# Kernel optimization log

Measured on AMD Instinct MI355X. Metric: run time of the kernel, lower is better.

The kernel has to match this reference:

```python
import jax, jax.numpy as jnp
import numpy as np

EPS = 1e-12          # matches torch F.normalize eps
NOW = 3600.0         # fixed 'current time'; timestamps are in [0,1)
TIME_DECAY = 3600.0  # temporal decay constant from the module

def setup_inputs() -> dict:
    key = jax.random.key(0)
    k1, k2, k3, k4, k5 = jax.random.split(key, 5)
    M, D, S = 100000, 768, 2
    return {
        "query_features": jax.random.normal(k1, (D,), dtype=jnp.float32),
        "location": jax.random.normal(k2, (S,), dtype=jnp.float32),
        "memory_features": jax.random.normal(k3, (M, D), dtype=jnp.float32),
        "memory_locations": jax.random.normal(k4, (M, S), dtype=jnp.float32),
        "memory_metadata": jax.random.uniform(k5, (M, 4), dtype=jnp.float32),
        "k": 5,
    }

def reference(query_features, location, memory_features, memory_locations, memory_metadata, k):
    # --- cosine similarity: normalize query and memory rows (F.normalize semantics) ---
    q_norm = query_features / jnp.maximum(jnp.linalg.norm(query_features), EPS)      # [D]
    m_norms = jnp.maximum(jnp.linalg.norm(memory_features, axis=1, keepdims=True), EPS)
    m_norm = memory_features / m_norms                                               # [M, D]
    sim_scores = m_norm @ q_norm                                                     # [M] GEMV

    # --- spatial score: 1 / (1 + euclidean distance to query location) ---
    dists = jnp.linalg.norm(memory_locations - location[None, :], axis=1)            # [M]
    spatial_scores = 1.0 / (1.0 + dists)

    # --- temporal score: exp(-age / 3600) ---
    strengths = memory_metadata[:, 0]
    timestamps = memory_metadata[:, 1]
    ages = NOW - timestamps
    temporal_scores = jnp.exp(-ages / TIME_DECAY)

    combined = (0.5 * sim_scores + 0.3 * spatial_scores + 0.2 * temporal_scores) * strengths

    top_scores, top_indices = jax.lax.top_k(combined, k)
    return top_scores, top_indices
```

## Files before the change

kernel.cpp:

```cpp
#include <hip/hip_runtime.h>
#include <math.h>

#define EPS   1e-12f
#define NOW_T 3600.0f
#define TDEC  3600.0f
#define K     5
#define D     768
#define GRID  2048

__device__ __forceinline__ void consider(float (&v)[K], int (&ix)[K], float s, int i)
{
    if (s > v[K - 1]) {
        int j = K - 1;
        #pragma unroll
        for (int t = K - 1; t > 0; --t) {
            if (v[t - 1] < s) { v[t] = v[t - 1]; ix[t] = ix[t - 1]; j = t - 1; }
        }
        v[j] = s; ix[j] = i;
    }
}

__global__ __launch_bounds__(256) void score_topk_kernel(
    const float* __restrict__ q,
    const float* __restrict__ loc,
    const float* __restrict__ feat,
    const float* __restrict__ mloc,
    const float* __restrict__ meta,
    float* __restrict__ cand_val,
    int*   __restrict__ cand_idx,
    int M)
{
    const int tid = threadIdx.x;
    const int c   = tid & 15;
    const int g   = tid >> 4;

    const float* qp = q + c * 4;
    float4 qv[12];
    float qss = 0.f;
    #pragma unroll
    for (int j = 0; j < 12; ++j) {
        qv[j] = *(const float4*)(qp + j * 64);
        qss = fmaf(qv[j].x, qv[j].x, qss);
        qss = fmaf(qv[j].y, qv[j].y, qss);
        qss = fmaf(qv[j].z, qv[j].z, qss);
        qss = fmaf(qv[j].w, qv[j].w, qss);
    }
    #pragma unroll
    for (int m = 1; m < 16; m <<= 1) qss += __shfl_xor(qss, m);
    const float inv_qn = 1.0f / fmaxf(sqrtf(qss), EPS);

    const float lx = loc[0];
    const float ly = loc[1];

    float v[K]; int ix[K];
    #pragma unroll
    for (int j = 0; j < K; ++j) { v[j] = -INFINITY; ix[j] = -1; }

    for (int base = blockIdx.x * 16; base < M; base += GRID * 16) {
        const int row = base + g;
        float dot = 0.f, ss = 0.f;
        if (row < M) {
            const float* r = feat + (size_t)row * D + c * 4;
            #pragma unroll
            for (int j = 0; j < 12; ++j) {
                float4 f = *(const float4*)(r + j * 64);
                dot = fmaf(f.x, qv[j].x, dot); ss = fmaf(f.x, f.x, ss);
                dot = fmaf(f.y, qv[j].y, dot); ss = fmaf(f.y, f.y, ss);
                dot = fmaf(f.z, qv[j].z, dot); ss = fmaf(f.z, f.z, ss);
                dot = fmaf(f.w, qv[j].w, dot); ss = fmaf(f.w, f.w, ss);
            }
        }
        #pragma unroll
        for (int m = 1; m < 16; m <<= 1) {
            dot += __shfl_xor(dot, m);
            ss  += __shfl_xor(ss,  m);
        }
        if (row < M && c == 0) {
            float sim = dot * inv_qn / fmaxf(sqrtf(ss), EPS);
            float2 ml = *(const float2*)(mloc + (size_t)row * 2);
            float4 md = *(const float4*)(meta + (size_t)row * 4);
            float dx = ml.x - lx, dy = ml.y - ly;
            float dist = sqrtf(dx * dx + dy * dy);
            float spatial  = 1.0f / (1.0f + dist);
            float temporal = expf((md.y - NOW_T) / TDEC);
            float s = (0.5f * sim + 0.3f * spatial + 0.2f * temporal) * md.x;
            consider(v, ix, s, row);
        }
    }

    __shared__ float sv[16 * K];
    __shared__ int   si[16 * K];
    if (c == 0) {
        #pragma unroll
        for (int j = 0; j < K; ++j) { sv[g * K + j] = v[j]; si[g * K + j] = ix[j]; }
    }
    __syncthreads();
    if (tid == 0) {
        float bv[K]; int bi[K];
        #pragma unroll
        for (int j = 0; j < K; ++j) { bv[j] = -INFINITY; bi[j] = -1; }
        for (int t = 0; t < 16 * K; ++t) consider(bv, bi, sv[t], si[t]);
        #pragma unroll
        for (int j = 0; j < K; ++j) {
            cand_val[blockIdx.x * K + j] = bv[j];
            cand_idx[blockIdx.x * K + j] = bi[j];
        }
    }
}

__global__ __launch_bounds__(1024) void merge_kernel(
    const float* __restrict__ cand_val, const int* __restrict__ cand_idx,
    int N, float* __restrict__ out)
{
    __shared__ float s_val[1024 * K];
    __shared__ int   s_idx[1024 * K];

    const int tid = threadIdx.x;
    float v[K]; int ix[K];
    #pragma unroll
    for (int j = 0; j < K; ++j) { v[j] = -INFINITY; ix[j] = -1; }

    for (int i = tid; i < N; i += 1024)
        consider(v, ix, cand_val[i], cand_idx[i]);

    #pragma unroll
    for (int j = 0; j < K; ++j) { s_val[tid * K + j] = v[j]; s_idx[tid * K + j] = ix[j]; }
    __syncthreads();

    for (int sz = 1024 >> 1; sz >= 1; sz >>= 1) {
        if (tid < sz) {
            const float* pv = &s_val[(tid + sz) * K];
            const int*   pi = &s_idx[(tid + sz) * K];
            float mv[K]; int mi[K];
            int a = 0, b = 0;
            #pragma unroll
            for (int j = 0; j < K; ++j) {
                bool takeA = (b >= K) || (a < K && v[a] >= pv[b]);
                if (takeA) { mv[j] = v[a];  mi[j] = ix[a]; ++a; }
                else       { mv[j] = pv[b]; mi[j] = pi[b]; ++b; }
            }
            #pragma unroll
            for (int j = 0; j < K; ++j) {
                v[j] = mv[j]; ix[j] = mi[j];
                s_val[tid * K + j] = v[j]; s_idx[tid * K + j] = ix[j];
            }
        }
        __syncthreads();
    }

    if (tid == 0) {
        #pragma unroll
        for (int j = 0; j < K; ++j) {
            out[j]     = v[j];
            out[K + j] = (float)ix[j];
        }
    }
}

extern "C" void kernel_launch(void* const* d_in, const int* in_sizes, int n_in,
                              void* d_out, int out_size, void* d_ws, size_t ws_size,
                              hipStream_t stream) {
    const float* q    = (const float*)d_in[0];
    const float* loc  = (const float*)d_in[1];
    const float* feat = (const float*)d_in[2];
    const float* mloc = (const float*)d_in[3];
    const float* meta = (const float*)d_in[4];
    const int M = in_sizes[2] / D;

    float* cand_val = (float*)d_ws;
    int*   cand_idx = (int*)((char*)d_ws + GRID * K * sizeof(float));

    score_topk_kernel<<<GRID, 256, 0, stream>>>(q, loc, feat, mloc, meta,
                                                cand_val, cand_idx, M);
    merge_kernel<<<1, 1024, 0, stream>>>(cand_val, cand_idx, GRID * K, (float*)d_out);
}
```

Before: 434.3 us.

## Fuse merge into scoring kernel via last-block atomic, contiguous row ranges, nontemporal loads

Folds the separate single-block merge kernel into the scoring kernel. Each block bumps an atomic counter when it finishes, and the last block to finish merges all candidates. Each block now scans a contiguous range of rows instead of a grid-strided set, and feature rows are read with nontemporal loads. The aim is to drop the second kernel launch and its dependency gap and to improve streaming from DRAM. In exchange it adds a memset per call and a serial merge tail on one 256-thread block.

After: 465.9 us. +7.3%, slower.

```diff
diff --git a/kernel.cpp b/kernel.cpp
--- a/kernel.cpp
+++ b/kernel.cpp
@@ -7,6 +7,8 @@
 #define K     5
 #define D     768
 #define GRID  2048
+
+typedef float vfloat4 __attribute__((ext_vector_type(4)));
 
 __device__ __forceinline__ void consider(float (&v)[K], int (&ix)[K], float s, int i)
 {
@@ -20,7 +22,7 @@
     }
 }
 
-__global__ __launch_bounds__(256) void score_topk_kernel(
+__global__ __launch_bounds__(256) void fused_kernel(
     const float* __restrict__ q,
     const float* __restrict__ loc,
     const float* __restrict__ feat,
@@ -28,6 +30,8 @@
     const float* __restrict__ meta,
     float* __restrict__ cand_val,
     int*   __restrict__ cand_idx,
+    unsigned* __restrict__ done_ctr,
+    float* __restrict__ out,
     int M)
 {
     const int tid = threadIdx.x;
@@ -35,11 +39,11 @@
     const int g   = tid >> 4;
 
     const float* qp = q + c * 4;
-    float4 qv[12];
+    vfloat4 qv[12];
     float qss = 0.f;
     #pragma unroll
     for (int j = 0; j < 12; ++j) {
-        qv[j] = *(const float4*)(qp + j * 64);
+        qv[j] = *(const vfloat4*)(qp + j * 64);
         qss = fmaf(qv[j].x, qv[j].x, qss);
         qss = fmaf(qv[j].y, qv[j].y, qss);
         qss = fmaf(qv[j].z, qv[j].z, qss);
@@ -52,18 +56,24 @@
     const float lx = loc[0];
     const float ly = loc[1];
 
+    const int per   = M / GRID;
+    const int rem   = M - per * GRID;
+    const int start = blockIdx.x * per + min((int)blockIdx.x, rem);
+    const int count = per + (blockIdx.x < rem ? 1 : 0);
+    const int end   = start + count;
+
     float v[K]; int ix[K];
     #pragma unroll
     for (int j = 0; j < K; ++j) { v[j] = -INFINITY; ix[j] = -1; }
 
-    for (int base = blockIdx.x * 16; base < M; base += GRID * 16) {
+    for (int base = start; base < end; base += 16) {
         const int row = base + g;
         float dot = 0.f, ss = 0.f;
-        if (row < M) {
+        if (row < end) {
             const float* r = feat + (size_t)row * D + c * 4;
             #pragma unroll
             for (int j = 0; j < 12; ++j) {
-                float4 f = *(const float4*)(r + j * 64);
+                vfloat4 f = __builtin_nontemporal_load((const vfloat4*)(r + j * 64));
                 dot = fmaf(f.x, qv[j].x, dot); ss = fmaf(f.x, f.x, ss);
                 dot = fmaf(f.y, qv[j].y, dot); ss = fmaf(f.y, f.y, ss);
                 dot = fmaf(f.z, qv[j].z, dot); ss = fmaf(f.z, f.z, ss);
@@ -75,7 +85,7 @@
             dot += __shfl_xor(dot, m);
             ss  += __shfl_xor(ss,  m);
         }
-        if (row < M && c == 0) {
+        if (row < end && c == 0) {
             float sim = dot * inv_qn / fmaxf(sqrtf(ss), EPS);
             float2 ml = *(const float2*)(mloc + (size_t)row * 2);
             float4 md = *(const float4*)(meta + (size_t)row * 4);
@@ -88,8 +98,10 @@
         }
     }
 
-    __shared__ float sv[16 * K];
-    __shared__ int   si[16 * K];
+    __shared__ float sv[256 * K];
+    __shared__ int   si[256 * K];
+    __shared__ bool  amLast;
+
     if (c == 0) {
         #pragma unroll
         for (int j = 0; j < K; ++j) { sv[g * K + j] = v[j]; si[g * K + j] = ix[j]; }
@@ -105,44 +117,40 @@
             cand_val[blockIdx.x * K + j] = bv[j];
             cand_idx[blockIdx.x * K + j] = bi[j];
         }
+        __threadfence();
+        unsigned prev = atomicAdd(done_ctr, 1u);
+        amLast = (prev == GRID - 1);
     }
-}
+    __syncthreads();
+    if (!amLast) return;
 
-__global__ __launch_bounds__(1024) void merge_kernel(
-    const float* __restrict__ cand_val, const int* __restrict__ cand_idx,
-    int N, float* __restrict__ out)
-{
-    __shared__ float s_val[1024 * K];
-    __shared__ int   s_idx[1024 * K];
-
-    const int tid = threadIdx.x;
-    float v[K]; int ix[K];
+    __threadfence();
+    float mv2[K]; int mi2[K];
     #pragma unroll
-    for (int j = 0; j < K; ++j) { v[j] = -INFINITY; ix[j] = -1; }
-
-    for (int i = tid; i < N; i += 1024)
-        consider(v, ix, cand_val[i], cand_idx[i]);
+    for (int j = 0; j < K; ++j) { mv2[j] = -INFINITY; mi2[j] = -1; }
+    for (int i = tid; i < GRID * K; i += 256)
+        consider(mv2, mi2, cand_val[i], cand_idx[i]);
 
     #pragma unroll
-    for (int j = 0; j < K; ++j) { s_val[tid * K + j] = v[j]; s_idx[tid * K + j] = ix[j]; }
+    for (int j = 0; j < K; ++j) { sv[tid * K + j] = mv2[j]; si[tid * K + j] = mi2[j]; }
     __syncthreads();
 
-    for (int sz = 1024 >> 1; sz >= 1; sz >>= 1) {
+    for (int sz = 128; sz >= 1; sz >>= 1) {
         if (tid < sz) {
-            const float* pv = &s_val[(tid + sz) * K];
-            const int*   pi = &s_idx[(tid + sz) * K];
-            float mv[K]; int mi[K];
+            const float* pv = &sv[(tid + sz) * K];
+            const int*   pi = &si[(tid + sz) * K];
+            float tv[K]; int ti[K];
             int a = 0, b = 0;
             #pragma unroll
             for (int j = 0; j < K; ++j) {
-                bool takeA = (b >= K) || (a < K && v[a] >= pv[b]);
-                if (takeA) { mv[j] = v[a];  mi[j] = ix[a]; ++a; }
-                else       { mv[j] = pv[b]; mi[j] = pi[b]; ++b; }
+                bool takeA = (b >= K) || (a < K && mv2[a] >= pv[b]);
+                if (takeA) { tv[j] = mv2[a]; ti[j] = mi2[a]; ++a; }
+                else       { tv[j] = pv[b];  ti[j] = pi[b];  ++b; }
             }
             #pragma unroll
             for (int j = 0; j < K; ++j) {
-                v[j] = mv[j]; ix[j] = mi[j];
-                s_val[tid * K + j] = v[j]; s_idx[tid * K + j] = ix[j];
+                mv2[j] = tv[j]; mi2[j] = ti[j];
+                sv[tid * K + j] = tv[j]; si[tid * K + j] = ti[j];
             }
         }
         __syncthreads();
@@ -151,8 +159,8 @@
     if (tid == 0) {
         #pragma unroll
         for (int j = 0; j < K; ++j) {
-            out[j]     = v[j];
-            out[K + j] = (float)ix[j];
+            out[j]     = mv2[j];
+            out[K + j] = (float)mi2[j];
         }
     }
 }
@@ -167,10 +175,12 @@
     const float* meta = (const float*)d_in[4];
     const int M = in_sizes[2] / D;
 
-    float* cand_val = (float*)d_ws;
-    int*   cand_idx = (int*)((char*)d_ws + GRID * K * sizeof(float));
+    float*    cand_val = (float*)d_ws;
+    int*      cand_idx = (int*)((char*)d_ws + GRID * K * sizeof(float));
+    unsigned* done_ctr = (unsigned*)((char*)d_ws + 2 * GRID * K * sizeof(float));
 
-    score_topk_kernel<<<GRID, 256, 0, stream>>>(q, loc, feat, mloc, meta,
-                                                cand_val, cand_idx, M);
-    merge_kernel<<<1, 1024, 0, stream>>>(cand_val, cand_idx, GRID * K, (float*)d_out);
+    hipMemsetAsync(done_ctr, 0, sizeof(unsigned), stream);
+    fused_kernel<<<GRID, 256, 0, stream>>>(q, loc, feat, mloc, meta,
+                                           cand_val, cand_idx, done_ctr,
+                                           (float*)d_out, M);
 }
```
